# Kernel tuning notes

Hardware: AMD Instinct MI355X
Metric: run time of the kernel (lower is better)

Reference implementation:

```python
import jax, jax.numpy as jnp
import numpy as np

ANCHORS = jnp.array([[1.3221, 1.73145], [3.19275, 4.00944], [5.05587, 8.09892],
                     [9.47112, 4.84053], [11.2364, 10.0071]], dtype=jnp.float32)
NUM_ANCHORS = 5
NUM_CLASSES = 20
MAX_BOXES = 50
NOOBJECT_SCALE = 1.0
OBJECT_SCALE = 5.0
COORD_SCALE = 1.0
CLASS_SCALE = 1.0
SIL_THRESH = 0.6


def iou_cwh(b1, b2):
    # boxes as (cx, cy, w, h); matches repo bbox_ious(x1y1x2y2=False)
    x1, y1, w1, h1 = b1[..., 0], b1[..., 1], b1[..., 2], b1[..., 3]
    x2, y2, w2, h2 = b2[..., 0], b2[..., 1], b2[..., 2], b2[..., 3]
    uw = jnp.maximum(x1 + w1 * 0.5, x2 + w2 * 0.5) - jnp.minimum(x1 - w1 * 0.5, x2 - w2 * 0.5)
    uh = jnp.maximum(y1 + h1 * 0.5, y2 + h2 * 0.5) - jnp.minimum(y1 - h1 * 0.5, y2 - h2 * 0.5)
    cw = w1 + w2 - uw
    ch = h1 + h2 - uh
    inter = jnp.where((cw <= 0) | (ch <= 0), 0.0, cw * ch)
    return inter / (w1 * h1 + w2 * h2 - inter)


def setup_inputs() -> dict:
    key = jax.random.key(0)
    k1, k2, k3, k4 = jax.random.split(key, 4)
    nB = 64
    output = jax.random.normal(k1, (nB, NUM_ANCHORS * (5 + NUM_CLASSES), 38, 38), dtype=jnp.float32)
    # target layout per box: (class, x, y, w, h), all normalized; x>0 marks a valid box
    cls_col = jax.random.randint(k2, (nB, MAX_BOXES, 1), 0, NUM_CLASSES).astype(jnp.float32)
    xy = jax.random.uniform(k3, (nB, MAX_BOXES, 2), minval=0.05, maxval=0.95)
    wh = jax.random.uniform(k4, (nB, MAX_BOXES, 2), minval=0.02, maxval=0.3)
    target = jnp.concatenate([cls_col, xy, wh], axis=-1).reshape(nB, MAX_BOXES * 5)
    return {"output": output, "target": target}


def region_loss(output, target):
    nB = output.shape[0]
    nA, nC = NUM_ANCHORS, NUM_CLASSES
    nH, nW = output.shape[2], output.shape[3]
    out = output.reshape(nB, nA, 5 + nC, nH, nW)
    x = jax.nn.sigmoid(out[:, :, 0])
    y = jax.nn.sigmoid(out[:, :, 1])
    w = out[:, :, 2]
    h = out[:, :, 3]
    conf = jax.nn.sigmoid(out[:, :, 4])
    # [nB,nA,nC,nH,nW] -> [nB*nA*nH*nW, nC] (matches torch transpose/view order)
    cls_logits = jnp.transpose(out[:, :, 5:], (0, 1, 3, 4, 2)).reshape(-1, nC)

    sg = jax.lax.stop_gradient
    aw, ah = ANCHORS[:, 0], ANCHORS[:, 1]
    grid_x = jnp.arange(nW, dtype=jnp.float32)[None, None, None, :]
    grid_y = jnp.arange(nH, dtype=jnp.float32)[None, None, :, None]
    px = sg(x) + grid_x
    py = sg(y) + grid_y
    pw = jnp.exp(sg(w)) * aw[None, :, None, None]
    ph = jnp.exp(sg(h)) * ah[None, :, None, None]
    pred_boxes = jnp.stack([px, py, pw, ph], axis=-1)  # [nB,nA,nH,nW,4]

    # ---- build_targets (vectorized) ----
    tgt = sg(target).reshape(nB, MAX_BOXES, 5)
    gcls = tgt[:, :, 0]
    gx = tgt[:, :, 1] * nW
    gy = tgt[:, :, 2] * nH
    gw = tgt[:, :, 3] * nW
    gh = tgt[:, :, 4] * nH
    # loop breaks at first x==0 -> cumulative validity
    valid = jnp.cumprod((tgt[:, :, 1] != 0).astype(jnp.int32), axis=1).astype(bool)

    # silence conf_mask where any-GT IoU > thresh
    pb_flat = pred_boxes.reshape(nB, nA * nH * nW, 4)
    gt_boxes = jnp.stack([gx, gy, gw, gh], axis=-1)  # [nB,50,4]
    ious = iou_cwh(pb_flat[:, :, None, :], gt_boxes[:, None, :, :])  # [nB,nAnc,50]
    ious = jnp.where(valid[:, None, :], ious, 0.0)
    max_iou = jnp.max(ious, axis=2)
    conf_mask = jnp.where(max_iou > SIL_THRESH, 0.0, NOOBJECT_SCALE).reshape(nB, nA, nH, nW)

    # seen < 12800 defaults
    shp = (nB, nA, nH, nW)
    coord_mask = jnp.ones(shp, jnp.float32)
    tx = jnp.full(shp, 0.5, jnp.float32)
    ty = jnp.full(shp, 0.5, jnp.float32)
    tw = jnp.zeros(shp, jnp.float32)
    th = jnp.zeros(shp, jnp.float32)
    tconf = jnp.zeros(shp, jnp.float32)
    tcls = jnp.zeros(shp, jnp.float32)
    cls_mask = jnp.zeros(shp, jnp.float32)

    # best anchor per GT by (0,0,w,h) IoU; argmax keeps first max like the strict '>' loop
    zA = jnp.zeros_like(aw)
    anchor_boxes = jnp.stack([zA, zA, aw, ah], axis=-1)  # [nA,4]
    zg = jnp.zeros_like(gw)
    gt_wh = jnp.stack([zg, zg, gw, gh], axis=-1)  # [nB,50,4]
    a_iou = iou_cwh(gt_wh[:, :, None, :], anchor_boxes[None, None, :, :])  # [nB,50,nA]
    best_n = jnp.argmax(a_iou, axis=2)  # [nB,50]

    gi = jnp.clip(gx.astype(jnp.int32), 0, nW - 1)
    gj = jnp.clip(gy.astype(jnp.int32), 0, nH - 1)
    aw_b = aw[best_n]
    ah_b = ah[best_n]
    tx_v = gx - gi.astype(jnp.float32)
    ty_v = gy - gj.astype(jnp.float32)
    tw_v = jnp.log(gw / aw_b)
    th_v = jnp.log(gh / ah_b)
    b_ix = jnp.arange(nB)
    pred_at = pred_boxes[b_ix[:, None], best_n, gj, gi]  # [nB,50,4]
    iou_gt = iou_cwh(gt_boxes, pred_at)  # [nB,50]

    def step(carry, t):
        cm, clm, tx_, ty_, tw_, th_, tcf, tcl = carry
        bsel = jnp.where(valid[:, t], b_ix, nB)  # out-of-bounds -> dropped
        n, j, i = best_n[:, t], gj[:, t], gi[:, t]
        st = lambda a, v: a.at[bsel, n, j, i].set(v, mode='drop')
        cm = st(cm, jnp.full((nB,), OBJECT_SCALE, jnp.float32))
        clm = st(clm, jnp.ones((nB,), jnp.float32))
        tx_ = st(tx_, tx_v[:, t])
        ty_ = st(ty_, ty_v[:, t])
        tw_ = st(tw_, tw_v[:, t])
        th_ = st(th_, th_v[:, t])
        tcf = st(tcf, iou_gt[:, t])
        tcl = st(tcl, gcls[:, t])
        return (cm, clm, tx_, ty_, tw_, th_, tcf, tcl), None

    init = (conf_mask, cls_mask, tx, ty, tw, th, tconf, tcls)
    (conf_mask, cls_mask, tx, ty, tw, th, tconf, tcls), _ = jax.lax.scan(
        step, init, jnp.arange(MAX_BOXES))

    # ---- losses ----
    cmf = jnp.sqrt(conf_mask)
    loss_x = COORD_SCALE * jnp.sum((x * coord_mask - tx * coord_mask) ** 2) / 2.0
    loss_y = COORD_SCALE * jnp.sum((y * coord_mask - ty * coord_mask) ** 2) / 2.0
    loss_w = COORD_SCALE * jnp.sum((w * coord_mask - tw * coord_mask) ** 2) / 2.0
    loss_h = COORD_SCALE * jnp.sum((h * coord_mask - th * coord_mask) ** 2) / 2.0
    loss_conf = jnp.sum((conf * cmf - tconf * cmf) ** 2) / 2.0
    logp = jax.nn.log_softmax(cls_logits, axis=-1)
    labels = tcls.reshape(-1).astype(jnp.int32)
    ce = -jnp.take_along_axis(logp, labels[:, None], axis=1)[:, 0]
    loss_cls = CLASS_SCALE * jnp.sum(ce * cls_mask.reshape(-1))
    return loss_x + loss_y + loss_w + loss_h + loss_conf + loss_cls


def reference(output, target):
    return region_loss(output, target)
```

## Files before the change

### kernel.cpp

```cpp
#include <hip/hip_runtime.h>
#include <math.h>

#define NA 5
#define NC 20
#define NH 38
#define NW 38
#define MAX_BOXES 50
#define SPAT (NH * NW)
#define CELLS_PER_B (NA * SPAT)
#define TPB 256
#define CELLS_PER_T 2
#define CPB (TPB * CELLS_PER_T)
#define GX ((CELLS_PER_B + CPB - 1) / CPB)
#define GXP (GX + 1)
#define OBJECT_SCALE 5.0f
#define NOOBJECT_SCALE 1.0f

__constant__ float c_aw[NA]  = {1.3221f, 3.19275f, 5.05587f, 9.47112f, 11.2364f};
__constant__ float c_ah[NA]  = {1.73145f, 4.00944f, 8.09892f, 4.84053f, 10.0071f};
__constant__ float c_iaw[NA] = {1.f/1.3221f, 1.f/3.19275f, 1.f/5.05587f, 1.f/9.47112f, 1.f/11.2364f};
__constant__ float c_iah[NA] = {1.f/1.73145f, 1.f/4.00944f, 1.f/8.09892f, 1.f/4.84053f, 1.f/10.0071f};

__device__ __forceinline__ float fexp(float v) { return __expf(v); }
__device__ __forceinline__ float flog(float v) { return __logf(v); }
__device__ __forceinline__ float frcp(float v) { return __builtin_amdgcn_rcpf(v); }
__device__ __forceinline__ float fsig(float v) { return frcp(1.f + __expf(-v)); }

__device__ __forceinline__ float iou_fast(float x1, float y1, float w1, float h1,
                                          float x2, float y2, float w2, float h2) {
  float uw = fmaxf(x1 + w1 * 0.5f, x2 + w2 * 0.5f) - fminf(x1 - w1 * 0.5f, x2 - w2 * 0.5f);
  float uh = fmaxf(y1 + h1 * 0.5f, y2 + h2 * 0.5f) - fminf(y1 - h1 * 0.5f, y2 - h2 * 0.5f);
  float cw = w1 + w2 - uw;
  float ch = h1 + h2 - uh;
  float inter = (cw <= 0.f || ch <= 0.f) ? 0.f : cw * ch;
  return inter * frcp(w1 * h1 + w2 * h2 - inter);
}

__device__ __forceinline__ float iou_wh_exact(float w1, float h1, float w2, float h2) {
  float uw = fmaxf(w1 * 0.5f, w2 * 0.5f) - fminf(-w1 * 0.5f, -w2 * 0.5f);
  float uh = fmaxf(h1 * 0.5f, h2 * 0.5f) - fminf(-h1 * 0.5f, -h2 * 0.5f);
  float cw = w1 + w2 - uw;
  float ch = h1 + h2 - uh;
  float inter = (cw <= 0.f || ch <= 0.f) ? 0.f : cw * ch;
  return inter / (w1 * h1 + w2 * h2 - inter);
}

__global__ __launch_bounds__(TPB) void fused_kernel(
    const float* __restrict__ out, const float* __restrict__ target,
    float* __restrict__ partials) {
  const int b = blockIdx.y;
  const int tid = threadIdx.x;

  __shared__ float4 sb_lo[MAX_BOXES];
  __shared__ float  sb_ag[MAX_BOXES];
  __shared__ float  s_red[TPB / 64];

  if (blockIdx.x == GX) {
    const int t = tid;
    const bool w0 = (tid < 64);
    float cls = 0.f, x = 0.f, y = 0.f, w = 0.f, h = 0.f;
    float gx = 0.f, gy = 0.f, gw = 0.f, gh = 0.f;
    bool winner = false;
    int best = 0, gi = 0, gj = 0;
    if (w0) {
      if (t < MAX_BOXES) {
        const float* tg = target + (size_t)(b * MAX_BOXES + t) * 5;
        cls = tg[0]; x = tg[1]; y = tg[2]; w = tg[3]; h = tg[4];
      }
      unsigned long long nz = __ballot(t < MAX_BOXES && x != 0.f);
      unsigned long long low = (t < 63) ? ((1ull << (t + 1)) - 1ull) : ~0ull;
      bool valid = (t < MAX_BOXES) && ((nz & low) == low);
      gx = x * NW; gy = y * NH; gw = w * NW; gh = h * NH;

      float bestiou = -1.f;
#pragma unroll
      for (int a2 = 0; a2 < NA; ++a2) {
        float aiou = iou_wh_exact(gw, gh, c_aw[a2], c_ah[a2]);
        if (aiou > bestiou) { bestiou = aiou; best = a2; }
      }
      gi = min(max((int)gx, 0), NW - 1);
      gj = min(max((int)gy, 0), NH - 1);
      int cell = best * SPAT + gj * NW + gi;

      unsigned long long vm = __ballot(valid);
      winner = valid;
      for (int tp = 0; tp < MAX_BOXES; ++tp) {
        int c2 = __shfl(cell, tp);
        if (tp > t && ((vm >> tp) & 1ull) && c2 == cell) winner = false;
      }
      if (t < MAX_BOXES) {
        if (valid) {
          sb_lo[t] = make_float4(gx - gw * 0.5f, gx + gw * 0.5f, gy - gh * 0.5f, gy + gh * 0.5f);
          sb_ag[t] = 0.375f * (gw * gh);
        } else {
          sb_lo[t] = make_float4(1e30f, 1e30f, 1e30f, 1e30f);
          sb_ag[t] = 0.f;
        }
      }
    }
    __syncthreads();

    float d = 0.f;
    if (w0 && winner) {
      const float* bp = out + ((size_t)(b * NA + best) * 25) * SPAT + gj * NW + gi;
      float v0 = bp[0], v1 = bp[SPAT], v2 = bp[2 * SPAT], v3 = bp[3 * SPAT], v4 = bp[4 * SPAT];
      float xs = fsig(v0), ys = fsig(v1), cs = fsig(v4);
      float pw = fexp(v2) * c_aw[best], ph = fexp(v3) * c_ah[best];
      float px = xs + (float)gi, py = ys + (float)gj;
      float plx = px - pw * 0.5f, phx = px + pw * 0.5f;
      float ply = py - ph * 0.5f, phy = py + ph * 0.5f;
      float ap = 0.375f * (pw * ph);

      float msc = -1e30f;
      for (int t2 = 0; t2 < MAX_BOXES; ++t2) {
        float4 l2 = sb_lo[t2];
        float cw = fminf(phx, l2.y) - fmaxf(plx, l2.x);
        float ch = fminf(phy, l2.w) - fmaxf(ply, l2.z);
        cw = fmaxf(cw, 0.f);
        msc = fmaxf(msc, fmaf(cw, ch, -sb_ag[t2]));
      }
      float cmask_def = (msc > ap) ? 0.f : NOOBJECT_SCALE;
      float xd = xs - 0.5f, yd = ys - 0.5f;
      float D = 0.5f * (xd * xd + yd * yd + v2 * v2 + v3 * v3 + cmask_def * (cs * cs));

      float txv = gx - (float)gi, tyv = gy - (float)gj;
      float twv = flog(gw * c_iaw[best]), thv = flog(gh * c_iah[best]);
      float tconf = iou_fast(gx, gy, gw, gh, px, py, pw, ph);
      float dx = xs - txv, dy = ys - tyv, dwv = v2 - twv, dhv = v3 - thv, dc = cs - tconf;

      int label = (int)cls;
      const float* cb = bp + 5 * SPAT;
      float vv[NC];
#pragma unroll
      for (int c = 0; c < NC; ++c) vv[c] = cb[c * SPAT];
      float m = -1e30f, lv = 0.f;
#pragma unroll
      for (int c = 0; c < NC; ++c) { if (c == label) lv = vv[c]; m = fmaxf(m, vv[c]); }
      float ssum = 0.f;
#pragma unroll
      for (int c = 0; c < NC; ++c) ssum += fexp(vv[c] - m);
      float ce = (m + flog(ssum)) - lv;

      float W = 0.5f * (dx * dx + dy * dy + dwv * dwv + dhv * dhv +
                        OBJECT_SCALE * (dc * dc)) + ce;
      d = W - D;
    }
    if (w0) {
      for (int o = 32; o > 0; o >>= 1) d += __shfl_down(d, o, 64);
      if (tid == 0) partials[(size_t)b * GXP + GX] = d;
    }
    return;
  }

  const int s0 = blockIdx.x * CPB;

  bool ok[CELLS_PER_T];
  float v0[CELLS_PER_T], v1[CELLS_PER_T], v2[CELLS_PER_T], v3[CELLS_PER_T], v4[CELLS_PER_T];
  float fi[CELLS_PER_T], fj[CELLS_PER_T], paw[CELLS_PER_T], pah[CELLS_PER_T];
#pragma unroll
  for (int q = 0; q < CELLS_PER_T; ++q) {
    int s = s0 + q * TPB + tid;
    ok[q] = (s < CELLS_PER_B);
    int sc = ok[q] ? s : 0;
    unsigned a = (unsigned)sc / SPAT;
    unsigned r = (unsigned)sc - a * SPAT;
    unsigned j = r / NW, i = r - j * NW;
    fi[q] = (float)i; fj[q] = (float)j;
    paw[q] = c_aw[a]; pah[q] = c_ah[a];
    const float* bp = out + ((size_t)(b * NA + a) * 25) * SPAT + r;
    v0[q] = bp[0];
    v1[q] = bp[SPAT];
    v2[q] = bp[2 * SPAT];
    v3[q] = bp[3 * SPAT];
    v4[q] = bp[4 * SPAT];
  }

  if (tid < 64) {
    const int t = tid;
    float x = 0.f, y = 0.f, w = 0.f, h = 0.f;
    if (t < MAX_BOXES) {
      const float* tg = target + (size_t)(b * MAX_BOXES + t) * 5;
      x = tg[1]; y = tg[2]; w = tg[3]; h = tg[4];
    }
    unsigned long long nz = __ballot(t < MAX_BOXES && x != 0.f);
    unsigned long long low = (t < 63) ? ((1ull << (t + 1)) - 1ull) : ~0ull;
    bool valid = (t < MAX_BOXES) && ((nz & low) == low);
    float gx = x * NW, gy = y * NH, gw = w * NW, gh = h * NH;
    if (t < MAX_BOXES) {
      if (valid) {
        sb_lo[t] = make_float4(gx - gw * 0.5f, gx + gw * 0.5f, gy - gh * 0.5f, gy + gh * 0.5f);
        sb_ag[t] = 0.375f * (gw * gh);
      } else {
        sb_lo[t] = make_float4(1e30f, 1e30f, 1e30f, 1e30f);
        sb_ag[t] = 0.f;
      }
    }
  }

  float xs[CELLS_PER_T], ys[CELLS_PER_T], cs[CELLS_PER_T];
  float plx[CELLS_PER_T], phx[CELLS_PER_T], ply[CELLS_PER_T], phy[CELLS_PER_T];
  float ap[CELLS_PER_T], msc[CELLS_PER_T];
#pragma unroll
  for (int q = 0; q < CELLS_PER_T; ++q) {
    xs[q] = fsig(v0[q]);
    ys[q] = fsig(v1[q]);
    cs[q] = fsig(v4[q]);
    float pw = fexp(v2[q]) * paw[q], ph = fexp(v3[q]) * pah[q];
    float px = xs[q] + fi[q], py = ys[q] + fj[q];
    plx[q] = px - pw * 0.5f; phx[q] = px + pw * 0.5f;
    ply[q] = py - ph * 0.5f; phy[q] = py + ph * 0.5f;
    ap[q] = 0.375f * (pw * ph);
    msc[q] = -1e30f;
  }
  __syncthreads();

#pragma unroll
  for (int c0 = 0; c0 < MAX_BOXES; c0 += 10) {
    float4 bl[10]; float bag[10];
#pragma unroll
    for (int u = 0; u < 10; ++u) { bl[u] = sb_lo[c0 + u]; bag[u] = sb_ag[c0 + u]; }
#pragma unroll
    for (int u = 0; u < 10; ++u) {
#pragma unroll
      for (int q = 0; q < CELLS_PER_T; ++q) {
        float cw = fminf(phx[q], bl[u].y) - fmaxf(plx[q], bl[u].x);
        float ch = fminf(phy[q], bl[u].w) - fmaxf(ply[q], bl[u].z);
        cw = fmaxf(cw, 0.f);
        msc[q] = fmaxf(msc[q], fmaf(cw, ch, -bag[u]));
      }
    }
  }

  float acc = 0.f;
#pragma unroll
  for (int q = 0; q < CELLS_PER_T; ++q) {
    if (!ok[q]) continue;
    float cmask = (msc[q] > ap[q]) ? 0.f : NOOBJECT_SCALE;
    float xd = xs[q] - 0.5f, yd = ys[q] - 0.5f;
    acc += 0.5f * (xd * xd + yd * yd + v2[q] * v2[q] + v3[q] * v3[q] +
                   cmask * (cs[q] * cs[q]));
  }

  for (int o = 32; o > 0; o >>= 1) acc += __shfl_down(acc, o, 64);
  int wid = tid >> 6, lane = tid & 63;
  if (lane == 0) s_red[wid] = acc;
  __syncthreads();
  if (tid == 0) {
    float v = 0.f;
#pragma unroll
    for (int wdx = 0; wdx < TPB / 64; ++wdx) v += s_red[wdx];
    partials[(size_t)b * GXP + blockIdx.x] = v;
  }
}

__global__ __launch_bounds__(256) void reduce_kernel(
    const float* __restrict__ vals, int n, float* __restrict__ outv) {
  float acc = 0.f;
  for (int i = threadIdx.x; i < n; i += 256) acc += vals[i];
  for (int o = 32; o > 0; o >>= 1) acc += __shfl_down(acc, o, 64);
  __shared__ float s_red[4];
  int wid = threadIdx.x >> 6, lane = threadIdx.x & 63;
  if (lane == 0) s_red[wid] = acc;
  __syncthreads();
  if (threadIdx.x == 0) outv[0] = s_red[0] + s_red[1] + s_red[2] + s_red[3];
}

extern "C" void kernel_launch(void* const* d_in, const int* in_sizes, int n_in,
                              void* d_out, int out_size, void* d_ws, size_t ws_size,
                              hipStream_t stream) {
  const float* out = (const float*)d_in[0];
  const float* target = (const float*)d_in[1];
  int nB = in_sizes[0] / (NA * (5 + NC) * SPAT);

  float* partials = (float*)d_ws;

  hipLaunchKernelGGL(fused_kernel, dim3(GXP, nB), dim3(TPB), 0, stream,
                     out, target, partials);
  hipLaunchKernelGGL(reduce_kernel, dim3(1), dim3(256), 0, stream,
                     partials, GXP * nB, (float*)d_out);
}
```

Measured before the change: 116.7 us.

## Use single-wavefront blocks with one cell per thread and drop LDS reduction

Replaces 256-thread blocks that each handle two cells per thread with 64-thread single-wavefront blocks that handle one cell per thread. The block-level shared-memory reduction goes away, and the special target block moves to index 0. This greatly raises the block count, so every block now rebuilds the 50-box table from global memory. The aim is better occupancy and latency hiding at the cost of more redundant box-setup work and more partial sums for the reduce kernel.

```diff
diff --git a/kernel.cpp b/kernel.cpp
--- a/kernel.cpp
+++ b/kernel.cpp
@@ -8,11 +8,9 @@
 #define MAX_BOXES 50
 #define SPAT (NH * NW)
 #define CELLS_PER_B (NA * SPAT)
-#define TPB 256
-#define CELLS_PER_T 2
-#define CPB (TPB * CELLS_PER_T)
-#define GX ((CELLS_PER_B + CPB - 1) / CPB)
-#define GXP (GX + 1)
+#define TPB 64
+#define BLOCKS_MAIN ((CELLS_PER_B + TPB - 1) / TPB)
+#define GXP (BLOCKS_MAIN + 1)
 #define OBJECT_SCALE 5.0f
 #define NOOBJECT_SCALE 1.0f
 
@@ -49,59 +47,51 @@
     const float* __restrict__ out, const float* __restrict__ target,
     float* __restrict__ partials) {
   const int b = blockIdx.y;
-  const int tid = threadIdx.x;
+  const int t = threadIdx.x;
 
   __shared__ float4 sb_lo[MAX_BOXES];
   __shared__ float  sb_ag[MAX_BOXES];
-  __shared__ float  s_red[TPB / 64];
-
-  if (blockIdx.x == GX) {
-    const int t = tid;
-    const bool w0 = (tid < 64);
+
+  if (blockIdx.x == 0) {
     float cls = 0.f, x = 0.f, y = 0.f, w = 0.f, h = 0.f;
-    float gx = 0.f, gy = 0.f, gw = 0.f, gh = 0.f;
-    bool winner = false;
-    int best = 0, gi = 0, gj = 0;
-    if (w0) {
-      if (t < MAX_BOXES) {
-        const float* tg = target + (size_t)(b * MAX_BOXES + t) * 5;
-        cls = tg[0]; x = tg[1]; y = tg[2]; w = tg[3]; h = tg[4];
-      }
-      unsigned long long nz = __ballot(t < MAX_BOXES && x != 0.f);
-      unsigned long long low = (t < 63) ? ((1ull << (t + 1)) - 1ull) : ~0ull;
-      bool valid = (t < MAX_BOXES) && ((nz & low) == low);
-      gx = x * NW; gy = y * NH; gw = w * NW; gh = h * NH;
-
-      float bestiou = -1.f;
-#pragma unroll
-      for (int a2 = 0; a2 < NA; ++a2) {
-        float aiou = iou_wh_exact(gw, gh, c_aw[a2], c_ah[a2]);
-        if (aiou > bestiou) { bestiou = aiou; best = a2; }
-      }
-      gi = min(max((int)gx, 0), NW - 1);
-      gj = min(max((int)gy, 0), NH - 1);
-      int cell = best * SPAT + gj * NW + gi;
-
-      unsigned long long vm = __ballot(valid);
-      winner = valid;
-      for (int tp = 0; tp < MAX_BOXES; ++tp) {
-        int c2 = __shfl(cell, tp);
-        if (tp > t && ((vm >> tp) & 1ull) && c2 == cell) winner = false;
-      }
-      if (t < MAX_BOXES) {
-        if (valid) {
-          sb_lo[t] = make_float4(gx - gw * 0.5f, gx + gw * 0.5f, gy - gh * 0.5f, gy + gh * 0.5f);
-          sb_ag[t] = 0.375f * (gw * gh);
-        } else {
-          sb_lo[t] = make_float4(1e30f, 1e30f, 1e30f, 1e30f);
-          sb_ag[t] = 0.f;
-        }
+    if (t < MAX_BOXES) {
+      const float* tg = target + (size_t)(b * MAX_BOXES + t) * 5;
+      cls = tg[0]; x = tg[1]; y = tg[2]; w = tg[3]; h = tg[4];
+    }
+    unsigned long long nz = __ballot(t < MAX_BOXES && x != 0.f);
+    unsigned long long low = (t < 63) ? ((1ull << (t + 1)) - 1ull) : ~0ull;
+    bool valid = (t < MAX_BOXES) && ((nz & low) == low);
+    float gx = x * NW, gy = y * NH, gw = w * NW, gh = h * NH;
+
+    int best = 0; float bestiou = -1.f;
+#pragma unroll
+    for (int a2 = 0; a2 < NA; ++a2) {
+      float aiou = iou_wh_exact(gw, gh, c_aw[a2], c_ah[a2]);
+      if (aiou > bestiou) { bestiou = aiou; best = a2; }
+    }
+    int gi = min(max((int)gx, 0), NW - 1);
+    int gj = min(max((int)gy, 0), NH - 1);
+    int cell = best * SPAT + gj * NW + gi;
+
+    unsigned long long vm = __ballot(valid);
+    bool winner = valid;
+    for (int tp = 0; tp < MAX_BOXES; ++tp) {
+      int c2 = __shfl(cell, tp);
+      if (tp > t && ((vm >> tp) & 1ull) && c2 == cell) winner = false;
+    }
+    if (t < MAX_BOXES) {
+      if (valid) {
+        sb_lo[t] = make_float4(gx - gw * 0.5f, gx + gw * 0.5f, gy - gh * 0.5f, gy + gh * 0.5f);
+        sb_ag[t] = 0.375f * (gw * gh);
+      } else {
+        sb_lo[t] = make_float4(1e30f, 1e30f, 1e30f, 1e30f);
+        sb_ag[t] = 0.f;
       }
     }
     __syncthreads();
 
     float d = 0.f;
-    if (w0 && winner) {
+    if (winner) {
       const float* bp = out + ((size_t)(b * NA + best) * 25) * SPAT + gj * NW + gi;
       float v0 = bp[0], v1 = bp[SPAT], v2 = bp[2 * SPAT], v3 = bp[3 * SPAT], v4 = bp[4 * SPAT];
       float xs = fsig(v0), ys = fsig(v1), cs = fsig(v4);
@@ -130,53 +120,37 @@
 
       int label = (int)cls;
       const float* cb = bp + 5 * SPAT;
-      float vv[NC];
-#pragma unroll
-      for (int c = 0; c < NC; ++c) vv[c] = cb[c * SPAT];
       float m = -1e30f, lv = 0.f;
-#pragma unroll
-      for (int c = 0; c < NC; ++c) { if (c == label) lv = vv[c]; m = fmaxf(m, vv[c]); }
+      for (int c = 0; c < NC; ++c) {
+        float vvc = cb[c * SPAT];
+        if (c == label) lv = vvc;
+        m = fmaxf(m, vvc);
+      }
       float ssum = 0.f;
-#pragma unroll
-      for (int c = 0; c < NC; ++c) ssum += fexp(vv[c] - m);
+      for (int c = 0; c < NC; ++c) ssum += fexp(cb[c * SPAT] - m);
       float ce = (m + flog(ssum)) - lv;
 
       float W = 0.5f * (dx * dx + dy * dy + dwv * dwv + dhv * dhv +
                         OBJECT_SCALE * (dc * dc)) + ce;
       d = W - D;
     }
-    if (w0) {
-      for (int o = 32; o > 0; o >>= 1) d += __shfl_down(d, o, 64);
-      if (tid == 0) partials[(size_t)b * GXP + GX] = d;
-    }
+    for (int o = 32; o > 0; o >>= 1) d += __shfl_down(d, o, 64);
+    if (t == 0) partials[(size_t)b * GXP] = d;
     return;
   }
 
-  const int s0 = blockIdx.x * CPB;
-
-  bool ok[CELLS_PER_T];
-  float v0[CELLS_PER_T], v1[CELLS_PER_T], v2[CELLS_PER_T], v3[CELLS_PER_T], v4[CELLS_PER_T];
-  float fi[CELLS_PER_T], fj[CELLS_PER_T], paw[CELLS_PER_T], pah[CELLS_PER_T];
-#pragma unroll
-  for (int q = 0; q < CELLS_PER_T; ++q) {
-    int s = s0 + q * TPB + tid;
-    ok[q] = (s < CELLS_PER_B);
-    int sc = ok[q] ? s : 0;
-    unsigned a = (unsigned)sc / SPAT;
-    unsigned r = (unsigned)sc - a * SPAT;
-    unsigned j = r / NW, i = r - j * NW;
-    fi[q] = (float)i; fj[q] = (float)j;
-    paw[q] = c_aw[a]; pah[q] = c_ah[a];
-    const float* bp = out + ((size_t)(b * NA + a) * 25) * SPAT + r;
-    v0[q] = bp[0];
-    v1[q] = bp[SPAT];
-    v2[q] = bp[2 * SPAT];
-    v3[q] = bp[3 * SPAT];
-    v4[q] = bp[4 * SPAT];
-  }
-
-  if (tid < 64) {
-    const int t = tid;
+  const int s = (blockIdx.x - 1) * TPB + t;
+  const bool ok = (s < CELLS_PER_B);
+  const int sc = ok ? s : 0;
+  unsigned a = (unsigned)sc / SPAT;
+  unsigned r = (unsigned)sc - a * SPAT;
+  unsigned j = r / NW, i = r - j * NW;
+  const float fi = (float)i, fj = (float)j;
+  const float paw = c_aw[a], pah = c_ah[a];
+  const float* bp = out + ((size_t)(b * NA + a) * 25) * SPAT + r;
+  float v0 = bp[0], v1 = bp[SPAT], v2 = bp[2 * SPAT], v3 = bp[3 * SPAT], v4 = bp[4 * SPAT];
+
+  {
     float x = 0.f, y = 0.f, w = 0.f, h = 0.f;
     if (t < MAX_BOXES) {
       const float* tg = target + (size_t)(b * MAX_BOXES + t) * 5;
@@ -197,60 +171,36 @@
     }
   }
 
-  float xs[CELLS_PER_T], ys[CELLS_PER_T], cs[CELLS_PER_T];
-  float plx[CELLS_PER_T], phx[CELLS_PER_T], ply[CELLS_PER_T], phy[CELLS_PER_T];
-  float ap[CELLS_PER_T], msc[CELLS_PER_T];
-#pragma unroll
-  for (int q = 0; q < CELLS_PER_T; ++q) {
-    xs[q] = fsig(v0[q]);
-    ys[q] = fsig(v1[q]);
-    cs[q] = fsig(v4[q]);
-    float pw = fexp(v2[q]) * paw[q], ph = fexp(v3[q]) * pah[q];
-    float px = xs[q] + fi[q], py = ys[q] + fj[q];
-    plx[q] = px - pw * 0.5f; phx[q] = px + pw * 0.5f;
-    ply[q] = py - ph * 0.5f; phy[q] = py + ph * 0.5f;
-    ap[q] = 0.375f * (pw * ph);
-    msc[q] = -1e30f;
-  }
+  float xs = fsig(v0), ys = fsig(v1), cs = fsig(v4);
+  float pw = fexp(v2) * paw, ph = fexp(v3) * pah;
+  float px = xs + fi, py = ys + fj;
+  float plx = px - pw * 0.5f, phx = px + pw * 0.5f;
+  float ply = py - ph * 0.5f, phy = py + ph * 0.5f;
+  float ap = 0.375f * (pw * ph), msc = -1e30f;
   __syncthreads();
 
 #pragma unroll
-  for (int c0 = 0; c0 < MAX_BOXES; c0 += 10) {
-    float4 bl[10]; float bag[10];
-#pragma unroll
-    for (int u = 0; u < 10; ++u) { bl[u] = sb_lo[c0 + u]; bag[u] = sb_ag[c0 + u]; }
-#pragma unroll
-    for (int u = 0; u < 10; ++u) {
-#pragma unroll
-      for (int q = 0; q < CELLS_PER_T; ++q) {
-        float cw = fminf(phx[q], bl[u].y) - fmaxf(plx[q], bl[u].x);
-        float ch = fminf(phy[q], bl[u].w) - fmaxf(ply[q], bl[u].z);
-        cw = fmaxf(cw, 0.f);
-        msc[q] = fmaxf(msc[q], fmaf(cw, ch, -bag[u]));
-      }
+  for (int c0 = 0; c0 < MAX_BOXES; c0 += 5) {
+    float4 bl[5]; float bag[5];
+#pragma unroll
+    for (int u = 0; u < 5; ++u) { bl[u] = sb_lo[c0 + u]; bag[u] = sb_ag[c0 + u]; }
+#pragma unroll
+    for (int u = 0; u < 5; ++u) {
+      float cw = fminf(phx, bl[u].y) - fmaxf(plx, bl[u].x);
+      float ch = fminf(phy, bl[u].w) - fmaxf(ply, bl[u].z);
+      cw = fmaxf(cw, 0.f);
+      msc = fmaxf(msc, fmaf(cw, ch, -bag[u]));
     }
   }
 
   float acc = 0.f;
-#pragma unroll
-  for (int q = 0; q < CELLS_PER_T; ++q) {
-    if (!ok[q]) continue;
-    float cmask = (msc[q] > ap[q]) ? 0.f : NOOBJECT_SCALE;
-    float xd = xs[q] - 0.5f, yd = ys[q] - 0.5f;
-    acc += 0.5f * (xd * xd + yd * yd + v2[q] * v2[q] + v3[q] * v3[q] +
-                   cmask * (cs[q] * cs[q]));
-  }
-
+  if (ok) {
+    float cmask = (msc > ap) ? 0.f : NOOBJECT_SCALE;
+    float xd = xs - 0.5f, yd = ys - 0.5f;
+    acc = 0.5f * (xd * xd + yd * yd + v2 * v2 + v3 * v3 + cmask * (cs * cs));
+  }
   for (int o = 32; o > 0; o >>= 1) acc += __shfl_down(acc, o, 64);
-  int wid = tid >> 6, lane = tid & 63;
-  if (lane == 0) s_red[wid] = acc;
-  __syncthreads();
-  if (tid == 0) {
-    float v = 0.f;
-#pragma unroll
-    for (int wdx = 0; wdx < TPB / 64; ++wdx) v += s_red[wdx];
-    partials[(size_t)b * GXP + blockIdx.x] = v;
-  }
+  if (t == 0) partials[(size_t)b * GXP + blockIdx.x] = acc;
 }
 
 __global__ __launch_bounds__(256) void reduce_kernel(
```

New measurement: 101.0 us. 1.16x faster.
